# Performance work log

Measured on AMD Instinct MI355X. Metric: run time of the kernel, lower is better.

The kernel has to match this reference:

```python
import jax, jax.numpy as jnp
import numpy as np

B, S, D = 4, 2048, 1024


def setup_inputs() -> dict:
    key = jax.random.key(0)
    ks = jax.random.split(key, 9)
    s = 1.0 / np.sqrt(D)
    return {
        "x": jax.random.normal(ks[0], (B, S, D), dtype=jnp.float32),
        "Wq": jax.random.normal(ks[1], (D, D), dtype=jnp.float32) * s,
        "bq": jnp.zeros((D,), dtype=jnp.float32),
        "Wk": jax.random.normal(ks[2], (D, D), dtype=jnp.float32) * s,
        "bk": jnp.zeros((D,), dtype=jnp.float32),
        "Wv": jax.random.normal(ks[3], (D, D), dtype=jnp.float32) * s,
        "bv": jnp.zeros((D,), dtype=jnp.float32),
        "Wo": jax.random.normal(ks[4], (D, D), dtype=jnp.float32) * s,
        "bo": jnp.zeros((D,), dtype=jnp.float32),
    }


def reference(x, Wq, bq, Wk, bk, Wv, bv, Wo, bo):
    # Projections: [B,S,D] @ [D,D] -> [B,S,D]
    q = jnp.einsum("bsd,de->bse", x, Wq) + bq
    k = jnp.einsum("bsd,de->bse", x, Wk) + bk
    v = jnp.einsum("bsd,de->bse", x, Wv) + bv
    # Unscaled single-head attention: scores [B,S,S]
    scores = jnp.einsum("bqd,bkd->bqk", q, k)
    dist = jax.nn.softmax(scores, axis=-1)
    attn = jnp.einsum("bqk,bkd->bqd", dist, v)
    # Output projection + residual
    return jnp.einsum("bsd,de->bse", attn, Wo) + bo + x
```

## Files before the change

kernel.cpp:

```cpp
#include <hip/hip_runtime.h>
#include <hip/hip_bf16.h>

#define DEVI __device__ __forceinline__

typedef __attribute__((ext_vector_type(8))) _Float16 f16x8;
typedef __attribute__((ext_vector_type(4))) float f32x4;
typedef __attribute__((ext_vector_type(4))) unsigned short us4;

#define VMW(N) asm volatile("s_waitcnt vmcnt(" #N ")" ::: "memory")
DEVI void sbar() {
  asm volatile("" ::: "memory");
  __builtin_amdgcn_s_barrier();
  asm volatile("" ::: "memory");
}

DEVI unsigned short f2h(float f) {
  union { _Float16 h; unsigned short u; } v;
  v.h = (_Float16)f;
  return v.u;
}

__global__ void __launch_bounds__(256) k_convert_f16(
    const float* __restrict__ x, unsigned short* __restrict__ o, int n4) {
  int i = blockIdx.x * 256 + threadIdx.x;
  if (i >= n4) return;
  float4 v = reinterpret_cast<const float4*>(x)[i];
  us4 h;
  h[0] = f2h(v.x); h[1] = f2h(v.y); h[2] = f2h(v.z); h[3] = f2h(v.w);
  reinterpret_cast<us4*>(o)[i] = h;
}

__global__ void __launch_bounds__(256) k_transpose_f16(
    const float* __restrict__ W, unsigned short* __restrict__ T, int n) {
  __shared__ float t[32][33];
  int tx = threadIdx.x & 31, ty = threadIdx.x >> 5;
  int n0 = blockIdx.x * 32, k0 = blockIdx.y * 32;
#pragma unroll
  for (int r = 0; r < 4; ++r)
    t[ty + r * 8][tx] = W[(size_t)(k0 + ty + r * 8) * n + n0 + tx];
  __syncthreads();
#pragma unroll
  for (int r = 0; r < 4; ++r) {
    int nn = n0 + ty + r * 8;
    T[(size_t)nn * n + k0 + tx] = f2h(t[tx][ty + r * 8]);
  }
}

DEVI void stageA(unsigned short* lbase, const unsigned short* g, int ldg, int tid) {
#pragma unroll
  for (int it = 0; it < 4; ++it) {
    int chunk = it * 512 + tid;
    int r = chunk >> 3, s = chunk & 7;
    int c = (s ^ (r & 7)) * 8;
    const unsigned short* gp = g + (size_t)r * ldg + c;
    unsigned short* lp = lbase + (it * 512 + (tid & ~63)) * 8;
    __builtin_amdgcn_global_load_lds(
        (const __attribute__((address_space(1))) unsigned int*)gp,
        (__attribute__((address_space(3))) unsigned int*)lp, 16, 0, 0);
  }
}
DEVI void stageB(unsigned short* lbase, const unsigned short* g, int ldg, int tid) {
#pragma unroll
  for (int it = 0; it < 2; ++it) {
    int chunk = it * 512 + tid;
    int r = chunk >> 3, s = chunk & 7;
    int c = (s ^ (r & 7)) * 8;
    const unsigned short* gp = g + (size_t)r * ldg + c;
    unsigned short* lp = lbase + (it * 512 + (tid & ~63)) * 8;
    __builtin_amdgcn_global_load_lds(
        (const __attribute__((address_space(1))) unsigned int*)gp,
        (__attribute__((address_space(3))) unsigned int*)lp, 16, 0, 0);
  }
}

DEVI f16x8 frag(const unsigned short* base, int row, int kk, int lr) {
  int slot = (kk * 4 + lr) ^ (row & 7);
  return *reinterpret_cast<const f16x8*>(base + row * 64 + slot * 8);
}

template <int EPI>
__global__ void __launch_bounds__(512, 2) k_gemm(
    const unsigned short* __restrict__ A, const unsigned short* __restrict__ B,
    int nt, int ldA, int ldB,
    size_t azs, size_t bzs, size_t czs,
    const float* __restrict__ b0, const float* __restrict__ b1,
    const float* __restrict__ b2, const float* __restrict__ resid,
    float* __restrict__ outF, unsigned short* __restrict__ o0,
    unsigned short* __restrict__ o1, unsigned short* __restrict__ o2, int ldc) {
  __shared__ unsigned short lds[3 * 24576];

  const int gx = gridDim.x, gy = gridDim.y;
  const int nwg = gx * gy * gridDim.z;
  const int l = (blockIdx.z * gy + blockIdx.y) * gx + blockIdx.x;
  const int nl = (l & 7) * (nwg >> 3) + (l >> 3);
  const int bx = nl % gx;
  const int rem = nl / gx;
  const int by = rem % gy;
  const int z = rem / gy;

  const int tid = threadIdx.x, lane = tid & 63, wid = tid >> 6;
  const int wr = (wid >> 1) * 64, wc = (wid & 1) * 64;
  const int lc = lane & 15, lr = lane >> 4;
  const size_t row0 = (size_t)bx * 256, col0 = (size_t)by * 128;

  const unsigned short* Ag = A + (size_t)z * azs + row0 * ldA;
  const unsigned short* Bg = B + (size_t)z * bzs + col0 * ldB;

  f32x4 acc[4][4] = {};

  stageA(lds, Ag, ldA, tid);
  stageB(lds + 16384, Bg, ldB, tid);
  stageA(lds + 24576, Ag + 64, ldA, tid);
  stageB(lds + 24576 + 16384, Bg + 64, ldB, tid);

  for (int t = 0; t < nt; ++t) {
    unsigned short* cur = lds + (t % 3) * 24576;
    if (t + 2 < nt) {
      unsigned short* nx = lds + ((t + 2) % 3) * 24576;
      stageA(nx, Ag + (size_t)(t + 2) * 64, ldA, tid);
      stageB(nx + 16384, Bg + (size_t)(t + 2) * 64, ldB, tid);
      VMW(12);
    } else if (t + 1 < nt) {
      VMW(6);
    } else {
      VMW(0);
    }
    sbar();
#pragma unroll
    for (int kk = 0; kk < 2; ++kk) {
      f16x8 af[4], bf[4];
#pragma unroll
      for (int i = 0; i < 4; ++i) {
        af[i] = frag(cur, wr + i * 16 + lc, kk, lr);
        bf[i] = frag(cur + 16384, wc + i * 16 + lc, kk, lr);
      }
#pragma unroll
      for (int mi = 0; mi < 4; ++mi)
#pragma unroll
        for (int ni = 0; ni < 4; ++ni)
          acc[mi][ni] = __builtin_amdgcn_mfma_f32_16x16x32_f16(af[mi], bf[ni], acc[mi][ni], 0, 0, 0);
    }
    sbar();
  }

#pragma unroll
  for (int mi = 0; mi < 4; ++mi) {
#pragma unroll
    for (int ni = 0; ni < 4; ++ni) {
      const int r0 = (int)row0 + wr + mi * 16 + lr * 4;
      const int c = (int)col0 + wc + ni * 16 + lc;
      f32x4 a = acc[mi][ni];
      if (EPI == 0) {
        const int sub = (int)(col0 >> 10);
        const int cc = c & 1023;
        if (sub == 0) {
          float b = b0[cc];
#pragma unroll
          for (int r = 0; r < 4; ++r)
            o0[(size_t)(r0 + r) * 1024 + cc] = f2h(a[r] + b);
        } else if (sub == 1) {
          float b = b1[cc];
#pragma unroll
          for (int r = 0; r < 4; ++r)
            o1[(size_t)(r0 + r) * 1024 + cc] = f2h(a[r] + b);
        } else {
          float b = b2[cc];
          us4 pk;
#pragma unroll
          for (int r = 0; r < 4; ++r) pk[r] = f2h(a[r] + b);
          *reinterpret_cast<us4*>(o2 + ((size_t)(r0 >> 11) * 1024 + cc) * 2048 + (r0 & 2047)) = pk;
        }
      } else if (EPI == 2) {
#pragma unroll
        for (int r = 0; r < 4; ++r)
          outF[(size_t)z * czs + (size_t)(r0 + r) * ldc + c] = a[r];
      } else if (EPI == 3) {
#pragma unroll
        for (int r = 0; r < 4; ++r)
          o0[(size_t)z * czs + (size_t)(r0 + r) * ldc + c] = f2h(a[r]);
      } else {
        float b = b0[c];
#pragma unroll
        for (int r = 0; r < 4; ++r) {
          size_t idx = (size_t)(r0 + r) * ldc + c;
          outF[idx] = a[r] + b + resid[idx];
        }
      }
    }
  }
}

__global__ void __launch_bounds__(256) k_softmax(
    const float* __restrict__ S, unsigned short* __restrict__ P) {
  __shared__ float red[4];
  const int row = blockIdx.x, tid = threadIdx.x;
  const int lane = tid & 63, wid = tid >> 6;
  const float* src = S + (size_t)row * 2048;
  float4 v0 = *reinterpret_cast<const float4*>(src + tid * 8);
  float4 v1 = *reinterpret_cast<const float4*>(src + tid * 8 + 4);
  float vv[8] = {v0.x, v0.y, v0.z, v0.w, v1.x, v1.y, v1.z, v1.w};
  float m = vv[0];
#pragma unroll
  for (int j = 1; j < 8; ++j) m = fmaxf(m, vv[j]);
#pragma unroll
  for (int o = 32; o > 0; o >>= 1) m = fmaxf(m, __shfl_xor(m, o));
  if (lane == 0) red[wid] = m;
  __syncthreads();
  m = fmaxf(fmaxf(red[0], red[1]), fmaxf(red[2], red[3]));
  __syncthreads();
  float e[8];
  float s = 0.f;
#pragma unroll
  for (int j = 0; j < 8; ++j) { e[j] = __expf(vv[j] - m); s += e[j]; }
#pragma unroll
  for (int o = 32; o > 0; o >>= 1) s += __shfl_xor(s, o);
  if (lane == 0) red[wid] = s;
  __syncthreads();
  s = red[0] + red[1] + red[2] + red[3];
  float inv = 1.0f / s;
  us4 p0, p1;
#pragma unroll
  for (int j = 0; j < 4; ++j) p0[j] = f2h(e[j] * inv);
#pragma unroll
  for (int j = 0; j < 4; ++j) p1[j] = f2h(e[j + 4] * inv);
  us4* dst = reinterpret_cast<us4*>(P + (size_t)row * 4096 + tid * 8);
  dst[0] = p0;
  dst[1] = p1;
}

extern "C" void kernel_launch(void* const* d_in, const int* in_sizes, int n_in,
                              void* d_out, int out_size, void* d_ws, size_t ws_size,
                              hipStream_t stream) {
  (void)in_sizes; (void)n_in; (void)out_size; (void)ws_size;
  const float* x  = (const float*)d_in[0];
  const float* Wq = (const float*)d_in[1];
  const float* bq = (const float*)d_in[2];
  const float* Wk = (const float*)d_in[3];
  const float* bk = (const float*)d_in[4];
  const float* Wv = (const float*)d_in[5];
  const float* bv = (const float*)d_in[6];
  const float* Wo = (const float*)d_in[7];
  const float* bo = (const float*)d_in[8];
  float* out = (float*)d_out;

  char* p = (char*)d_ws;
  auto take = [&](size_t bytes) {
    char* r = p;
    p += (bytes + 255) & ~(size_t)255;
    return r;
  };
  const size_t SD = (size_t)4 * 2048 * 1024;
  unsigned short* x_h   = (unsigned short*)take(SD * 2);
  unsigned short* q_h   = (unsigned short*)take(SD * 2);
  unsigned short* k_h   = (unsigned short*)take(SD * 2);
  unsigned short* WqkvT = (unsigned short*)take((size_t)3072 * 1024 * 2);
  unsigned short* WoT   = (unsigned short*)take((size_t)1024 * 1024 * 2);
  unsigned short* v_t   = (unsigned short*)take(SD * 2);
  unsigned short* attn  = (unsigned short*)take(SD * 2);
  const size_t SC_B = (size_t)2048 * 2048;
  float* scores = (float*)take(4 * SC_B * 4);

  dim3 blk(256), blk5(512);
  k_convert_f16<<<dim3(8192), blk, 0, stream>>>(x, x_h, (int)(SD / 4));
  k_transpose_f16<<<dim3(32, 32), blk, 0, stream>>>(Wq, WqkvT, 1024);
  k_transpose_f16<<<dim3(32, 32), blk, 0, stream>>>(Wk, WqkvT + (size_t)1024 * 1024, 1024);
  k_transpose_f16<<<dim3(32, 32), blk, 0, stream>>>(Wv, WqkvT + (size_t)2048 * 1024, 1024);
  k_transpose_f16<<<dim3(32, 32), blk, 0, stream>>>(Wo, WoT, 1024);

  k_gemm<0><<<dim3(32, 24, 1), blk5, 0, stream>>>(
      x_h, WqkvT, 16, 1024, 1024, 0, 0, 0,
      bq, bk, bv, nullptr, nullptr, q_h, k_h, v_t, 0);

  const size_t QZS = (size_t)2048 * 1024;
  const size_t VZS = (size_t)1024 * 2048;
  const size_t PZS = SC_B * 2;
  k_gemm<2><<<dim3(8, 16, 4), blk5, 0, stream>>>(
      q_h, k_h, 16, 1024, 1024, QZS, QZS, SC_B,
      nullptr, nullptr, nullptr, nullptr, scores, nullptr, nullptr, nullptr, 2048);
  k_softmax<<<dim3(8192), blk, 0, stream>>>(scores, (unsigned short*)scores);
  k_gemm<3><<<dim3(8, 8, 4), blk5, 0, stream>>>(
      (const unsigned short*)scores, v_t, 32, 4096, 2048, PZS, VZS, QZS,
      nullptr, nullptr, nullptr, nullptr, nullptr, attn, nullptr, nullptr, 1024);
  k_gemm<4><<<dim3(32, 8, 1), blk5, 0, stream>>>(
      attn, WoT, 16, 1024, 1024, 0, 0, 0,
      bo, nullptr, nullptr, x, out, nullptr, nullptr, nullptr, 1024);
}
```

Baseline: 232.3 us.

## Use 256x256 ping-pong GEMM for QKV/scores and small tiles for PV/out

Result: faster. 224.1 us (-3.5%).

```diff
diff --git a/kernel.cpp b/kernel.cpp
--- a/kernel.cpp
+++ b/kernel.cpp
@@ -46,48 +46,63 @@
   }
 }
 
-DEVI void stageA(unsigned short* lbase, const unsigned short* g, int ldg, int tid) {
-#pragma unroll
-  for (int it = 0; it < 4; ++it) {
-    int chunk = it * 512 + tid;
-    int r = chunk >> 3, s = chunk & 7;
-    int c = (s ^ (r & 7)) * 8;
-    const unsigned short* gp = g + (size_t)r * ldg + c;
-    unsigned short* lp = lbase + (it * 512 + (tid & ~63)) * 8;
-    __builtin_amdgcn_global_load_lds(
-        (const __attribute__((address_space(1))) unsigned int*)gp,
-        (__attribute__((address_space(3))) unsigned int*)lp, 16, 0, 0);
-  }
-}
-DEVI void stageB(unsigned short* lbase, const unsigned short* g, int ldg, int tid) {
+DEVI void gload16(const unsigned short* gp, unsigned short* lp) {
+  __builtin_amdgcn_global_load_lds(
+      (const __attribute__((address_space(1))) unsigned int*)gp,
+      (__attribute__((address_space(3))) unsigned int*)lp, 16, 0, 0);
+}
+
+DEVI f16x8 frag(const unsigned short* base, int row, int kk, int lr) {
+  int slot = (kk * 4 + lr) ^ (row & 7);
+  return *reinterpret_cast<const f16x8*>(base + row * 64 + slot * 8);
+}
+
+DEVI void stage_half(unsigned short* lbase, const unsigned short* g, int ldg, int tid) {
 #pragma unroll
   for (int it = 0; it < 2; ++it) {
     int chunk = it * 512 + tid;
     int r = chunk >> 3, s = chunk & 7;
     int c = (s ^ (r & 7)) * 8;
-    const unsigned short* gp = g + (size_t)r * ldg + c;
-    unsigned short* lp = lbase + (it * 512 + (tid & ~63)) * 8;
-    __builtin_amdgcn_global_load_lds(
-        (const __attribute__((address_space(1))) unsigned int*)gp,
-        (__attribute__((address_space(3))) unsigned int*)lp, 16, 0, 0);
-  }
-}
-
-DEVI f16x8 frag(const unsigned short* base, int row, int kk, int lr) {
-  int slot = (kk * 4 + lr) ^ (row & 7);
-  return *reinterpret_cast<const f16x8*>(base + row * 64 + slot * 8);
-}
+    gload16(g + (size_t)r * ldg + c, lbase + (it * 512 + (tid & ~63)) * 8);
+  }
+}
+
+#define PHASE(AB, BB, MI0, READB, STAGE_STMT, ENDVM)                          \
+  {                                                                           \
+    STAGE_STMT;                                                               \
+    if (READB) {                                                              \
+      _Pragma("unroll") for (int ni = 0; ni < 4; ++ni)                        \
+          _Pragma("unroll") for (int kk = 0; kk < 2; ++kk)                    \
+              b[ni][kk] = frag((BB), (wid & 1) * 64 + ni * 16 + lc, kk, lr);  \
+    }                                                                         \
+    f16x8 a00 = frag((AB), (MI0) * 16 + lc, 0, lr);                           \
+    f16x8 a01 = frag((AB), (MI0) * 16 + lc, 1, lr);                           \
+    f16x8 a10 = frag((AB), (MI0 + 1) * 16 + lc, 0, lr);                       \
+    f16x8 a11 = frag((AB), (MI0 + 1) * 16 + lc, 1, lr);                       \
+    sbar();                                                                   \
+    asm volatile("s_waitcnt lgkmcnt(0)" ::: "memory");                        \
+    __builtin_amdgcn_sched_barrier(0);                                        \
+    __builtin_amdgcn_s_setprio(1);                                            \
+    _Pragma("unroll") for (int ni = 0; ni < 4; ++ni) {                        \
+      acc[MI0][ni] = __builtin_amdgcn_mfma_f32_16x16x32_f16(a00, b[ni][0], acc[MI0][ni], 0, 0, 0);             \
+      acc[MI0][ni] = __builtin_amdgcn_mfma_f32_16x16x32_f16(a01, b[ni][1], acc[MI0][ni], 0, 0, 0);             \
+      acc[MI0 + 1][ni] = __builtin_amdgcn_mfma_f32_16x16x32_f16(a10, b[ni][0], acc[MI0 + 1][ni], 0, 0, 0);     \
+      acc[MI0 + 1][ni] = __builtin_amdgcn_mfma_f32_16x16x32_f16(a11, b[ni][1], acc[MI0 + 1][ni], 0, 0, 0);     \
+    }                                                                         \
+    __builtin_amdgcn_s_setprio(0);                                            \
+    ENDVM;                                                                    \
+    sbar();                                                                   \
+  }
 
 template <int EPI>
-__global__ void __launch_bounds__(512, 2) k_gemm(
+__global__ void __launch_bounds__(512, 1) k_gemm8(
     const unsigned short* __restrict__ A, const unsigned short* __restrict__ B,
-    int nt, int ldA, int ldB,
-    size_t azs, size_t bzs, size_t czs,
+    int nt2, int ldA, int ldB, size_t azs, size_t bzs, size_t czs,
     const float* __restrict__ b0, const float* __restrict__ b1,
-    const float* __restrict__ b2, const float* __restrict__ resid,
+    const float* __restrict__ b2,
     float* __restrict__ outF, unsigned short* __restrict__ o0,
     unsigned short* __restrict__ o1, unsigned short* __restrict__ o2, int ldc) {
-  __shared__ unsigned short lds[3 * 24576];
+  __shared__ __align__(16) unsigned short lds[65536];
 
   const int gx = gridDim.x, gy = gridDim.y;
   const int nwg = gx * gy * gridDim.z;
@@ -99,40 +114,157 @@
   const int z = rem / gy;
 
   const int tid = threadIdx.x, lane = tid & 63, wid = tid >> 6;
+  const int lc = lane & 15, lr = lane >> 4;
+  const int ha = wid >> 2;
+  const int hb = (wid & 3) >> 1;
+  const size_t row0 = (size_t)bx * 256, col0 = (size_t)by * 256;
+
+  unsigned short* SA00 = lds;
+  unsigned short* SA01 = lds + 8192;
+  unsigned short* SA10 = lds + 16384;
+  unsigned short* SA11 = lds + 24576;
+  unsigned short* SB00 = lds + 32768;
+  unsigned short* SB01 = lds + 40960;
+  unsigned short* SB10 = lds + 49152;
+  unsigned short* SB11 = lds + 57344;
+
+  const unsigned short* Ag0 = A + (size_t)z * azs + row0 * ldA;
+  const unsigned short* Ag1 = Ag0 + (size_t)128 * ldA;
+  const unsigned short* Bg0 = B + (size_t)z * bzs + col0 * ldB;
+  const unsigned short* Bg1 = Bg0 + (size_t)128 * ldB;
+
+  const unsigned short* Ab0 = SA00 + ha * 8192;
+  const unsigned short* Ab1 = SA10 + ha * 8192;
+  const unsigned short* Bb0 = SB00 + hb * 8192;
+  const unsigned short* Bb1 = SB10 + hb * 8192;
+
+  f32x4 acc[8][4] = {};
+  f16x8 b[4][2];
+
+  stage_half(SA00, Ag0, ldA, tid);
+  stage_half(SA01, Ag1, ldA, tid);
+  stage_half(SB00, Bg0, ldB, tid);
+  stage_half(SB01, Bg1, ldB, tid);
+  stage_half(SB10, Bg0 + 64, ldB, tid);
+  stage_half(SB11, Bg1 + 64, ldB, tid);
+  VMW(4);
+  sbar();
+
+  for (int t = 0; t < nt2; ++t) {
+    const int kb = t << 7;
+    const bool more = (t + 1 < nt2);
+    PHASE(Ab0, Bb0, 0, true,
+          { stage_half(SA10, Ag0 + kb + 64, ldA, tid);
+            stage_half(SA11, Ag1 + kb + 64, ldA, tid); },
+          {});
+    PHASE(Ab0, Bb0, 2, false,
+          { if (more) { stage_half(SB00, Bg0 + kb + 128, ldB, tid);
+                        stage_half(SB01, Bg1 + kb + 128, ldB, tid); } },
+          {});
+    PHASE(Ab0, Bb0, 4, false, {}, {});
+    PHASE(Ab0, Bb0, 6, false, {},
+          { if (more) { VMW(4); } else { VMW(0); } });
+    PHASE(Ab1, Bb1, 0, true,
+          { if (more) { stage_half(SA00, Ag0 + kb + 128, ldA, tid);
+                        stage_half(SA01, Ag1 + kb + 128, ldA, tid); } },
+          {});
+    PHASE(Ab1, Bb1, 2, false,
+          { if (more) { stage_half(SB10, Bg0 + kb + 192, ldB, tid);
+                        stage_half(SB11, Bg1 + kb + 192, ldB, tid); } },
+          {});
+    PHASE(Ab1, Bb1, 4, false, {}, {});
+    PHASE(Ab1, Bb1, 6, false, {},
+          { if (more) { VMW(4); } });
+  }
+
+#pragma unroll
+  for (int mi = 0; mi < 8; ++mi) {
+#pragma unroll
+    for (int ni = 0; ni < 4; ++ni) {
+      const int r0 = (int)row0 + (wid >> 2) * 128 + mi * 16 + lr * 4;
+      const int c = (int)col0 + (wid & 3) * 64 + ni * 16 + lc;
+      f32x4 a = acc[mi][ni];
+      if (EPI == 0) {
+        const int sub = c >> 10;
+        const int cc = c & 1023;
+        if (sub == 0) {
+          float bb = b0[cc];
+#pragma unroll
+          for (int r = 0; r < 4; ++r)
+            o0[(size_t)(r0 + r) * 1024 + cc] = f2h(a[r] + bb);
+        } else if (sub == 1) {
+          float bb = b1[cc];
+#pragma unroll
+          for (int r = 0; r < 4; ++r)
+            o1[(size_t)(r0 + r) * 1024 + cc] = f2h(a[r] + bb);
+        } else {
+          float bb = b2[cc];
+          us4 pk;
+#pragma unroll
+          for (int r = 0; r < 4; ++r) pk[r] = f2h(a[r] + bb);
+          *reinterpret_cast<us4*>(o2 + ((size_t)(r0 >> 11) * 1024 + cc) * 2048 + (r0 & 2047)) = pk;
+        }
+      } else {
+#pragma unroll
+        for (int r = 0; r < 4; ++r)
+          outF[(size_t)z * czs + (size_t)(r0 + r) * ldc + c] = a[r];
+      }
+    }
+  }
+}
+
+DEVI void stage_tile64s(unsigned short* lbase, const unsigned short* g, int ldg,
+                        int wid, int lane) {
+#pragma unroll
+  for (int it = 0; it < 4; ++it) {
+    int chunk = it * 256 + wid * 64 + lane;
+    int r = chunk >> 3, s = chunk & 7;
+    int c = (s ^ (r & 7)) * 8;
+    gload16(g + (size_t)r * ldg + c, lbase + (it * 256 + wid * 64) * 8);
+  }
+}
+
+template <int EPI>
+__global__ void __launch_bounds__(256, 4) k_gemm_s(
+    const unsigned short* __restrict__ A, const unsigned short* __restrict__ B,
+    int K, int ldA, int ldB,
+    size_t azs, size_t bzs, size_t czs,
+    const float* __restrict__ bias, const float* __restrict__ resid,
+    float* __restrict__ outF, unsigned short* __restrict__ outH, int ldc) {
+  __shared__ unsigned short lds[2 * 8192];
+  unsigned short* Alds = lds;
+  unsigned short* Blds = lds + 8192;
+
+  const int gx = gridDim.x, gy = gridDim.y;
+  const int nwg = gx * gy * gridDim.z;
+  const int l = (blockIdx.z * gy + blockIdx.y) * gx + blockIdx.x;
+  const int nl = (l & 7) * (nwg >> 3) + (l >> 3);
+  const int bx = nl % gx;
+  const int rem = nl / gx;
+  const int by = rem % gy;
+  const int z = rem / gy;
+
+  const int tid = threadIdx.x, lane = tid & 63, wid = tid >> 6;
   const int wr = (wid >> 1) * 64, wc = (wid & 1) * 64;
   const int lc = lane & 15, lr = lane >> 4;
-  const size_t row0 = (size_t)bx * 256, col0 = (size_t)by * 128;
+  const size_t row0 = (size_t)bx * 128, col0 = (size_t)by * 128;
 
   const unsigned short* Ag = A + (size_t)z * azs + row0 * ldA;
   const unsigned short* Bg = B + (size_t)z * bzs + col0 * ldB;
 
   f32x4 acc[4][4] = {};
 
-  stageA(lds, Ag, ldA, tid);
-  stageB(lds + 16384, Bg, ldB, tid);
-  stageA(lds + 24576, Ag + 64, ldA, tid);
-  stageB(lds + 24576 + 16384, Bg + 64, ldB, tid);
-
-  for (int t = 0; t < nt; ++t) {
-    unsigned short* cur = lds + (t % 3) * 24576;
-    if (t + 2 < nt) {
-      unsigned short* nx = lds + ((t + 2) % 3) * 24576;
-      stageA(nx, Ag + (size_t)(t + 2) * 64, ldA, tid);
-      stageB(nx + 16384, Bg + (size_t)(t + 2) * 64, ldB, tid);
-      VMW(12);
-    } else if (t + 1 < nt) {
-      VMW(6);
-    } else {
-      VMW(0);
-    }
-    sbar();
+  for (int k0 = 0; k0 < K; k0 += 64) {
+    stage_tile64s(Alds, Ag + k0, ldA, wid, lane);
+    stage_tile64s(Blds, Bg + k0, ldB, wid, lane);
+    __syncthreads();
 #pragma unroll
     for (int kk = 0; kk < 2; ++kk) {
       f16x8 af[4], bf[4];
 #pragma unroll
       for (int i = 0; i < 4; ++i) {
-        af[i] = frag(cur, wr + i * 16 + lc, kk, lr);
-        bf[i] = frag(cur + 16384, wc + i * 16 + lc, kk, lr);
+        af[i] = frag(Alds, wr + i * 16 + lc, kk, lr);
+        bf[i] = frag(Blds, wc + i * 16 + lc, kk, lr);
       }
 #pragma unroll
       for (int mi = 0; mi < 4; ++mi)
@@ -140,7 +272,7 @@
         for (int ni = 0; ni < 4; ++ni)
           acc[mi][ni] = __builtin_amdgcn_mfma_f32_16x16x32_f16(af[mi], bf[ni], acc[mi][ni], 0, 0, 0);
     }
-    sbar();
+    __syncthreads();
   }
 
 #pragma unroll
@@ -150,36 +282,12 @@
       const int r0 = (int)row0 + wr + mi * 16 + lr * 4;
       const int c = (int)col0 + wc + ni * 16 + lc;
       f32x4 a = acc[mi][ni];
-      if (EPI == 0) {
-        const int sub = (int)(col0 >> 10);
-        const int cc = c & 1023;
-        if (sub == 0) {
-          float b = b0[cc];
-#pragma unroll
-          for (int r = 0; r < 4; ++r)
-            o0[(size_t)(r0 + r) * 1024 + cc] = f2h(a[r] + b);
-        } else if (sub == 1) {
-          float b = b1[cc];
-#pragma unroll
-          for (int r = 0; r < 4; ++r)
-            o1[(size_t)(r0 + r) * 1024 + cc] = f2h(a[r] + b);
-        } else {
-          float b = b2[cc];
-          us4 pk;
-#pragma unroll
-          for (int r = 0; r < 4; ++r) pk[r] = f2h(a[r] + b);
-          *reinterpret_cast<us4*>(o2 + ((size_t)(r0 >> 11) * 1024 + cc) * 2048 + (r0 & 2047)) = pk;
-        }
-      } else if (EPI == 2) {
+      if (EPI == 3) {
 #pragma unroll
         for (int r = 0; r < 4; ++r)
-          outF[(size_t)z * czs + (size_t)(r0 + r) * ldc + c] = a[r];
-      } else if (EPI == 3) {
-#pragma unroll
-        for (int r = 0; r < 4; ++r)
-          o0[(size_t)z * czs + (size_t)(r0 + r) * ldc + c] = f2h(a[r]);
+          outH[(size_t)z * czs + (size_t)(r0 + r) * ldc + c] = f2h(a[r]);
       } else {
-        float b = b0[c];
+        float b = bias[c];
 #pragma unroll
         for (int r = 0; r < 4; ++r) {
           size_t idx = (size_t)(r0 + r) * ldc + c;
@@ -267,21 +375,21 @@
   k_transpose_f16<<<dim3(32, 32), blk, 0, stream>>>(Wv, WqkvT + (size_t)2048 * 1024, 1024);
   k_transpose_f16<<<dim3(32, 32), blk, 0, stream>>>(Wo, WoT, 1024);
 
-  k_gemm<0><<<dim3(32, 24, 1), blk5, 0, stream>>>(
-      x_h, WqkvT, 16, 1024, 1024, 0, 0, 0,
-      bq, bk, bv, nullptr, nullptr, q_h, k_h, v_t, 0);
+  k_gemm8<0><<<dim3(32, 12, 1), blk5, 0, stream>>>(
+      x_h, WqkvT, 8, 1024, 1024, 0, 0, 0,
+      bq, bk, bv, nullptr, q_h, k_h, v_t, 0);
 
   const size_t QZS = (size_t)2048 * 1024;
   const size_t VZS = (size_t)1024 * 2048;
   const size_t PZS = SC_B * 2;
-  k_gemm<2><<<dim3(8, 16, 4), blk5, 0, stream>>>(
-      q_h, k_h, 16, 1024, 1024, QZS, QZS, SC_B,
-      nullptr, nullptr, nullptr, nullptr, scores, nullptr, nullptr, nullptr, 2048);
+  k_gemm8<2><<<dim3(8, 8, 4), blk5, 0, stream>>>(
+      q_h, k_h, 8, 1024, 1024, QZS, QZS, SC_B,
+      nullptr, nullptr, nullptr, scores, nullptr, nullptr, nullptr, 2048);
   k_softmax<<<dim3(8192), blk, 0, stream>>>(scores, (unsigned short*)scores);
-  k_gemm<3><<<dim3(8, 8, 4), blk5, 0, stream>>>(
-      (const unsigned short*)scores, v_t, 32, 4096, 2048, PZS, VZS, QZS,
-      nullptr, nullptr, nullptr, nullptr, nullptr, attn, nullptr, nullptr, 1024);
-  k_gemm<4><<<dim3(32, 8, 1), blk5, 0, stream>>>(
-      attn, WoT, 16, 1024, 1024, 0, 0, 0,
-      bo, nullptr, nullptr, x, out, nullptr, nullptr, nullptr, 1024);
-}
+  k_gemm_s<3><<<dim3(16, 8, 4), blk, 0, stream>>>(
+      (const unsigned short*)scores, v_t, 2048, 4096, 2048, PZS, VZS, QZS,
+      nullptr, nullptr, nullptr, attn, 1024);
+  k_gemm_s<4><<<dim3(64, 8, 1), blk, 0, stream>>>(
+      attn, WoT, 1024, 1024, 1024, 0, 0, 0,
+      bo, x, out, nullptr, 1024);
+}
```
